# Kernel optimization log

Measured on AMD Instinct MI355X. Metric: run time of the kernel, lower is better.

Reference implementation:

```python
import jax, jax.numpy as jnp
import numpy as np

NUM_KIND = 4
V, Hh = 14, 6          # raw board
H, W = V - 2, Hh       # trimmed board 12x6
KS = 13                # full_kernel_size = max(12,6) -> odd 13
PAD = KS // 2
N_SQ = 100
LIN_IN = H * W         # 72


def _conv(x, w, b):
    # x: [N,1,H,W], w: [1,1,KS,KS], b: [1]
    y = jax.lax.conv_general_dilated(
        x, w, window_strides=(1, 1), padding=[(PAD, PAD), (PAD, PAD)],
        dimension_numbers=('NCHW', 'OIHW', 'NCHW'))
    return y + b[None, :, None, None]


def setup_inputs() -> dict:
    key = jax.random.key(0)
    ks = jax.random.split(key, 16)
    B = 65536
    dots = jax.random.randint(ks[0], (V, Hh, B), 0, NUM_KIND + 1, dtype=jnp.int32)
    std = 0.14
    def cw(k):
        return jax.random.normal(k, (1, 1, KS, KS), jnp.float32) * std
    def cb(k):
        return jax.random.normal(k, (1,), jnp.float32) * 0.05
    return {
        'dots_kind_matrix_3D': dots,
        'w_each': cw(ks[1]), 'b_each': cb(ks[2]),
        'w_not': cw(ks[3]), 'b_not': cb(ks[4]),
        'w_not2': cw(ks[5]), 'b_not2': cb(ks[6]),
        'w_empty': cw(ks[7]), 'b_empty': cb(ks[8]),
        'W1': jax.random.normal(ks[9], (N_SQ, LIN_IN), jnp.float32) * std,
        'b1': jax.random.normal(ks[10], (N_SQ,), jnp.float32) * 0.05,
        'W2': jax.random.normal(ks[11], (N_SQ, N_SQ), jnp.float32) * std,
        'b2': jax.random.normal(ks[12], (N_SQ,), jnp.float32) * 0.05,
        'W3': jax.random.normal(ks[13], (1, N_SQ), jnp.float32) * std,
        'b3': jax.random.normal(ks[14], (1,), jnp.float32) * 0.05,
    }


def _generate_linear_input(dots, w_each, b_each, w_not, b_not, w_not2, b_not2,
                           w_empty, b_empty):
    # trim last two rows, move batch axis first: [B,1,H,W]
    d = jnp.transpose(dots[:-2], (2, 0, 1))[:, None].astype(jnp.float32)
    B = d.shape[0]
    empty = _conv((d == 0).astype(jnp.float32), w_empty, b_empty)  # [B,1,H,W]

    # all kinds at once: masks [K,B,1,H,W]
    kinds = jnp.arange(1, NUM_KIND + 1, dtype=jnp.float32)
    masks = (d[None] == kinds[:, None, None, None, None]).astype(jnp.float32)

    mflat = masks.reshape(NUM_KIND * B, 1, H, W)
    ecv_log = _conv(mflat, w_each, b_each).reshape(NUM_KIND, B, 1, H, W)
    not_mat = jnp.where((masks + empty[None]) > 0, 0.0, 1.0)
    not_conv = _conv(not_mat.reshape(NUM_KIND * B, 1, H, W), w_not, b_not)
    not_conv = not_conv.reshape(NUM_KIND, B, 1, H, W)

    val = ecv_log + empty[None] - not_conv
    val = jnp.where(masks > 0, val, 0.0)
    all_color_value = jnp.sum(val, axis=0)  # [B,1,H,W]

    # second pass: sequential over kinds (carry feeds next iteration)
    def step(acv2, inp):
        ecm, ecv = inp  # [B,1,H,W]
        not2 = jnp.where((ecm + empty) > 0, 0.0, acv2)
        v = ecv + empty + _conv(not2, w_not2, b_not2)
        v = jnp.where(ecm > 0, v, 0.0)
        return acv2 + v, None

    acv2, _ = jax.lax.scan(step, all_color_value, (masks, ecv_log))
    return acv2.reshape(B, LIN_IN)


def reference(dots_kind_matrix_3D, w_each, b_each, w_not, b_not, w_not2, b_not2,
              w_empty, b_empty, W1, b1, W2, b2, W3, b3):
    x = _generate_linear_input(dots_kind_matrix_3D, w_each, b_each, w_not, b_not,
                               w_not2, b_not2, w_empty, b_empty)
    x = jax.nn.leaky_relu(x @ W1.T + b1, negative_slope=0.2)
    x = jax.nn.leaky_relu(x @ W2.T + b2, negative_slope=0.2)
    return x @ W3.T + b3  # [B,1]
```

## Files before the change

### kernel.cpp

```cpp
#include <hip/hip_runtime.h>

#define BN 65536
#define NT 256
#define NBB 64
#define NBLK (BN / NBB)

typedef unsigned int uint;
typedef unsigned short ushort;
typedef __attribute__((ext_vector_type(8))) short bf16x8;
typedef __attribute__((ext_vector_type(4))) float f32x4;

#define L_A  0
#define L_B  6400
#define L_B1 12800
#define L_B2 12912
#define L_W3 13024
#define L_TOT 13136

#define WS_W1 51200
#define WS_W2 69120
#define WS_TOT 94208
#define WS_MK_BYTE 188416

__device__ __forceinline__ uint f2b(float f){
  uint u = __float_as_uint(f);
  return (u + 0x7FFFu + ((u >> 16) & 1u)) >> 16;
}
__device__ __forceinline__ float b2f(uint h){ return __uint_as_float(h << 16); }
__device__ __forceinline__ uint dupb(float f){ uint b = f2b(f); return b | (b << 16); }

union BU { uint u[4]; bf16x8 v; };

__global__ __launch_bounds__(256) void k_setup(
    const float* __restrict__ w_each, const float* __restrict__ w_not,
    const float* __restrict__ w_not2, const float* __restrict__ w_empty,
    const float* __restrict__ W1, const float* __restrict__ W2,
    ushort* __restrict__ wsp)
{
  int id = blockIdx.x * 256 + threadIdx.x;
  if (id >= WS_TOT) return;
  float val = 0.f;
  int part;
  if (id < 51200) {
    int m = id / 12800, r = id % 12800;
    int fi = r >> 3, j = r & 7;
    int l = fi & 63, tk = fi >> 6;
    int ks = tk % 5, ti = tk / 5;
    int row = ti * 16 + (l & 15);
    int k = ks * 32 + (l >> 4) * 8 + j;
    int t = k >> 1; part = k & 1;
    if (row < 72 && t < 72) {
      int dr = t / 6 - row / 6 + 6, dc = t % 6 - row % 6 + 6;
      const float* w = m == 0 ? w_each : m == 1 ? w_not : m == 2 ? w_not2 : w_empty;
      if (dr >= 0 && dr < 13) val = w[dr * 13 + dc];
    }
  } else if (id < WS_W2) {
    int r = id - WS_W1;
    int fi = r >> 3, j = r & 7;
    int l = fi & 63, tk = fi >> 6;
    int ks = tk % 5, ti = tk / 5;
    int row = ti * 16 + (l & 15);
    int k = ks * 32 + (l >> 4) * 8 + j;
    int t = k >> 1; part = k & 1;
    if (row < 100 && t < 72) val = W1[row * 72 + t];
  } else {
    int r = id - WS_W2;
    int fi = r >> 3, j = r & 7;
    int l = fi & 63, tk = fi >> 6;
    int ks = tk % 7, ti = tk / 7;
    int row = ti * 16 + (l & 15);
    int k = ks * 32 + (l >> 4) * 8 + j;
    int t = k >> 1; part = k & 1;
    if (row < 100 && t < 100) val = W2[row * 100 + t];
  }
  uint h = f2b(val);
  if (part) { float rem = val - b2f(h); h = f2b(rem); }
  wsp[id] = (ushort)h;
}

__global__ __launch_bounds__(256) void k_masks(const int* __restrict__ dots,
                                               uint* __restrict__ MKg)
{
  int b = blockIdx.x * 256 + threadIdx.x;
  uint mk[5][3] = {};
#pragma unroll
  for (int c = 0; c < 72; ++c) {
    int v = dots[c * BN + b];
#pragma unroll
    for (int k = 0; k < 5; ++k)
      mk[k][c >> 5] |= (uint)(v == k) << (c & 31);
  }
#pragma unroll
  for (int k = 0; k < 5; ++k)
#pragma unroll
    for (int w = 0; w < 3; ++w)
      MKg[(k * 3 + w) * BN + b] = mk[k][w];
}

template<int NTK, int KW, int KS0, int NKS>
__device__ __forceinline__ void gstage(uint* afb, const ushort* __restrict__ wsp,
                                       int baseU16, int wid, int lane)
{
  const uint4* src = (const uint4*)(wsp + baseU16);
  constexpr int NIT = (NTK * 64 + NT - 1) / NT;
#pragma unroll
  for (int it = 0; it < NIT; ++it) {
    int tk = it * 4 + wid;
    if (tk < NTK) {
      int ksl = tk % NKS, ti = tk / NKS;
      const uint4* gp = src + (ti * KW + KS0 + ksl) * 64 + lane;
      uint4* lp = (uint4*)afb + tk * 64;
      __builtin_amdgcn_global_load_lds(
          (const __attribute__((address_space(1))) void*)gp,
          (__attribute__((address_space(3))) void*)lp, 16, 0, 0);
    }
  }
}

template<int NKS, int B0, int NBQ>
__device__ __forceinline__ void fcStep(const uint* sAF, const BU (&Bq)[NBQ],
                                       f32x4 (&Acc)[7], int lane)
{
  const bf16x8* AF = (const bf16x8*)sAF;
#pragma unroll
  for (int ti = 0; ti < 7; ++ti)
#pragma unroll
    for (int ksl = 0; ksl < NKS; ++ksl)
      Acc[ti] = __builtin_amdgcn_mfma_f32_16x16x32_bf16(
          AF[(ti * NKS + ksl) * 64 + lane], Bq[B0 + ksl].v, Acc[ti], 0, 0, 0);
}

__global__ __launch_bounds__(NT, 2) void k_main(
    const uint* __restrict__ MKg, const ushort* __restrict__ wsp,
    const float* __restrict__ b_each, const float* __restrict__ b_not,
    const float* __restrict__ b_not2, const float* __restrict__ b_empty,
    const float* __restrict__ b1, const float* __restrict__ b2,
    const float* __restrict__ W3, const float* __restrict__ b3,
    float* __restrict__ out)
{
  __shared__ uint sB[L_TOT];
  const int tid = threadIdx.x;
  const int wid = tid >> 6, lane = tid & 63;
  const int grp = lane >> 4;
  const int bl = wid * 16 + (lane & 15);
  const int gq = grp * 4;

  const float c_each = *b_each, c_not = *b_not, c_not2 = *b_not2, c_empty = *b_empty;
  const float c_b3 = *b3;

  if (tid < 112) {
    ((float*)(sB + L_B1))[tid] = (tid < 100) ? b1[tid] : 0.f;
    ((float*)(sB + L_B2))[tid] = (tid < 100) ? b2[tid] : 0.f;
    ((float*)(sB + L_W3))[tid] = (tid < 100) ? W3[tid] : 0.f;
  }
  gstage<25, 5, 0, 5>(sB + L_A, wsp, 3 * 12800, wid, lane);

  uint mkr[15];
  {
    const int gb = blockIdx.x * NBB + bl;
#pragma unroll
    for (int w = 0; w < 15; ++w) mkr[w] = MKg[w * BN + gb];
  }
  __syncthreads();

  f32x4 S5[5], A5[5];
  uint zws[5] = {0, 0, 0, 0, 0};

  gstage<25, 5, 0, 5>(sB + L_B, wsp, 0, wid, lane);
  {
    const bf16x8* AF = (const bf16x8*)(sB + L_A);
    BU Bv[5];
#pragma unroll
    for (int ks = 0; ks < 5; ++ks) {
      uint wv = mkr[0 * 3 + (ks >> 1)];
      int base = ((ks * 16) & 31) + gq;
#pragma unroll
      for (int q = 0; q < 4; ++q)
        Bv[ks].u[q] = ((wv >> (base + q)) & 1u) ? 0x3F803F80u : 0u;
    }
#pragma unroll
    for (int ti = 0; ti < 5; ++ti) {
      f32x4 d = {c_empty, c_empty, c_empty, c_empty};
#pragma unroll
      for (int ks = 0; ks < 5; ++ks)
        d = __builtin_amdgcn_mfma_f32_16x16x32_bf16(AF[(ti * 5 + ks) * 64 + lane], Bv[ks].v, d, 0, 0, 0);
      S5[ti] = d;
    }
  }
#pragma unroll
  for (int k = 1; k <= 4; ++k) {
#pragma unroll
    for (int ti = 0; ti < 5; ++ti) {
      uint wv = mkr[k * 3 + (ti >> 1)];
      int base = ((ti * 16) & 31) + gq;
#pragma unroll
      for (int r = 0; r < 4; ++r) {
        float mb = (float)((wv >> (base + r)) & 1u);
        if (S5[ti][r] + mb > 0.f) zws[ti] |= 1u << (r * 8 + (k - 1));
      }
    }
  }
  __syncthreads();

  gstage<25, 5, 0, 5>(sB + L_A, wsp, 1 * 12800, wid, lane);
  {
    const bf16x8* AF = (const bf16x8*)(sB + L_B);
#pragma unroll 1
    for (int k = 1; k <= 4; ++k) {
      BU Bv[5];
#pragma unroll
      for (int ks = 0; ks < 5; ++ks) {
        uint wv = mkr[k * 3 + (ks >> 1)];
        int base = ((ks * 16) & 31) + gq;
#pragma unroll
        for (int q = 0; q < 4; ++q)
          Bv[ks].u[q] = ((wv >> (base + q)) & 1u) ? 0x3F803F80u : 0u;
      }
#pragma unroll
      for (int ti = 0; ti < 5; ++ti) {
        f32x4 d = {c_each, c_each, c_each, c_each};
#pragma unroll
        for (int ks = 0; ks < 5; ++ks)
          d = __builtin_amdgcn_mfma_f32_16x16x32_bf16(AF[(ti * 5 + ks) * 64 + lane], Bv[ks].v, d, 0, 0, 0);
        uint wv = mkr[k * 3 + (ti >> 1)];
        int base = ((ti * 16) & 31) + gq;
#pragma unroll
        for (int r = 0; r < 4; ++r)
          if ((wv >> (base + r)) & 1u) S5[ti][r] += d[r];
      }
    }
  }
#pragma unroll
  for (int ti = 0; ti < 5; ++ti) {
    uint wv = mkr[0 * 3 + (ti >> 1)];
    int base = ((ti * 16) & 31) + gq;
#pragma unroll
    for (int r = 0; r < 4; ++r)
      A5[ti][r] = ((wv >> (base + r)) & 1u) ? 0.f : S5[ti][r];
  }
  __syncthreads();

  gstage<25, 5, 0, 5>(sB + L_B, wsp, 2 * 12800, wid, lane);
  {
    const bf16x8* AF = (const bf16x8*)(sB + L_A);
#pragma unroll 1
    for (int k = 1; k <= 4; ++k) {
      BU Bv[5];
#pragma unroll
      for (int ks = 0; ks < 5; ++ks) {
#pragma unroll
        for (int q = 0; q < 4; ++q)
          Bv[ks].u[q] = ((zws[ks] >> (q * 8 + (k - 1))) & 1u) ? 0u : 0x3F803F80u;
      }
#pragma unroll
      for (int ti = 0; ti < 5; ++ti) {
        f32x4 d = {c_not, c_not, c_not, c_not};
#pragma unroll
        for (int ks = 0; ks < 5; ++ks)
          d = __builtin_amdgcn_mfma_f32_16x16x32_bf16(AF[(ti * 5 + ks) * 64 + lane], Bv[ks].v, d, 0, 0, 0);
        uint wv = mkr[k * 3 + (ti >> 1)];
        int base = ((ti * 16) & 31) + gq;
#pragma unroll
        for (int r = 0; r < 4; ++r)
          if ((wv >> (base + r)) & 1u) A5[ti][r] -= d[r];
      }
    }
  }
  __syncthreads();

  gstage<21, 5, 0, 3>(sB + L_A, wsp, WS_W1, wid, lane);
  {
    const bf16x8* AF = (const bf16x8*)(sB + L_B);
#pragma unroll 1
    for (int k = 1; k <= 4; ++k) {
      BU Bv[5];
#pragma unroll
      for (int ks = 0; ks < 5; ++ks) {
#pragma unroll
        for (int q = 0; q < 4; ++q)
          Bv[ks].u[q] = ((zws[ks] >> (q * 8 + (k - 1))) & 1u) ? 0u : dupb(A5[ks][q]);
      }
#pragma unroll
      for (int ti = 0; ti < 5; ++ti) {
        f32x4 d = {c_not2, c_not2, c_not2, c_not2};
#pragma unroll
        for (int ks = 0; ks < 5; ++ks)
          d = __builtin_amdgcn_mfma_f32_16x16x32_bf16(AF[(ti * 5 + ks) * 64 + lane], Bv[ks].v, d, 0, 0, 0);
        uint wv = mkr[k * 3 + (ti >> 1)];
        int base = ((ti * 16) & 31) + gq;
#pragma unroll
        for (int r = 0; r < 4; ++r)
          if ((wv >> (base + r)) & 1u) A5[ti][r] += S5[ti][r] + d[r];
      }
    }
  }
  __syncthreads();

  BU Bx[5];
#pragma unroll
  for (int ks = 0; ks < 5; ++ks)
#pragma unroll
    for (int q = 0; q < 4; ++q) Bx[ks].u[q] = dupb(A5[ks][q]);
  f32x4 H[7];
#pragma unroll
  for (int ti = 0; ti < 7; ++ti) H[ti] = ((const f32x4*)(sB + L_B1))[ti * 4 + grp];

  gstage<14, 5, 3, 2>(sB + L_B, wsp, WS_W1, wid, lane);
  fcStep<3, 0>(sB + L_A, Bx, H, lane);
  __syncthreads();
  gstage<21, 7, 0, 3>(sB + L_A, wsp, WS_W2, wid, lane);
  fcStep<2, 3>(sB + L_B, Bx, H, lane);

  BU By[7];
#pragma unroll
  for (int ti = 0; ti < 7; ++ti) {
#pragma unroll
    for (int r = 0; r < 4; ++r) { float x = H[ti][r]; H[ti][r] = fmaxf(x, 0.2f * x); }
#pragma unroll
    for (int r = 0; r < 4; ++r) By[ti].u[r] = dupb(H[ti][r]);
  }
  f32x4 G[7];
#pragma unroll
  for (int ti = 0; ti < 7; ++ti) G[ti] = ((const f32x4*)(sB + L_B2))[ti * 4 + grp];
  __syncthreads();

  gstage<14, 7, 3, 2>(sB + L_B, wsp, WS_W2, wid, lane);
  fcStep<3, 0>(sB + L_A, By, G, lane);
  __syncthreads();
  gstage<14, 7, 5, 2>(sB + L_A, wsp, WS_W2, wid, lane);
  fcStep<2, 3>(sB + L_B, By, G, lane);
  __syncthreads();
  fcStep<2, 5>(sB + L_A, By, G, lane);

  float pd = 0.f;
#pragma unroll
  for (int ti = 0; ti < 7; ++ti) {
    f32x4 w3v = ((const f32x4*)(sB + L_W3))[ti * 4 + grp];
#pragma unroll
    for (int r = 0; r < 4; ++r) {
      float g = G[ti][r];
      g = fmaxf(g, 0.2f * g);
      pd = fmaf(w3v[r], g, pd);
    }
  }
  pd += __shfl_xor(pd, 16);
  pd += __shfl_xor(pd, 32);
  if (lane < 16) out[blockIdx.x * NBB + wid * 16 + lane] = pd + c_b3;
}

extern "C" void kernel_launch(void* const* d_in, const int* in_sizes, int n_in,
                              void* d_out, int out_size, void* d_ws, size_t ws_size,
                              hipStream_t stream)
{
  const int*   dots    = (const int*)d_in[0];
  const float* w_each  = (const float*)d_in[1];
  const float* b_each  = (const float*)d_in[2];
  const float* w_not   = (const float*)d_in[3];
  const float* b_not   = (const float*)d_in[4];
  const float* w_not2  = (const float*)d_in[5];
  const float* b_not2  = (const float*)d_in[6];
  const float* w_empty = (const float*)d_in[7];
  const float* b_empty = (const float*)d_in[8];
  const float* W1 = (const float*)d_in[9];
  const float* b1 = (const float*)d_in[10];
  const float* W2 = (const float*)d_in[11];
  const float* b2 = (const float*)d_in[12];
  const float* W3 = (const float*)d_in[13];
  const float* b3 = (const float*)d_in[14];

  (void)in_sizes; (void)n_in; (void)out_size; (void)ws_size;

  ushort* wsp = (ushort*)d_ws;
  uint*   MKg = (uint*)((char*)d_ws + WS_MK_BYTE);

  k_setup<<<(WS_TOT + 255) / 256, 256, 0, stream>>>(
      w_each, w_not, w_not2, w_empty, W1, W2, wsp);
  k_masks<<<BN / 256, 256, 0, stream>>>(dots, MKg);
  k_main<<<NBLK, NT, 0, stream>>>(
      MKg, wsp, b_each, b_not, b_not2, b_empty, b1, b2, W3, b3, (float*)d_out);
}
```

Measured before the change: 58.22 us.

## Merge prep kernels, skip structurally zero conv tiles, pair kinds, use hardware bf16 cvt

Fuses the weight-setup and mask-building kernels into one launch, removing a kernel launch and its gap. Skips MFMA calls for the two conv-weight tile blocks that are structurally zero given the 13x13 kernel on the 12x6 board. Processes kinds in pairs in the each-conv stage so each A fragment load feeds two MFMAs. Replaces the software round-to-nearest bf16 packing with the v_cvt_pk_bf16_f32 instruction, which may round slightly differently.

```diff
diff --git a/kernel.cpp b/kernel.cpp
--- a/kernel.cpp
+++ b/kernel.cpp
@@ -21,22 +21,47 @@
 #define WS_W2 69120
 #define WS_TOT 94208
 #define WS_MK_BYTE 188416
+#define SETUP_BLOCKS 368
+
+#define ZBLK(ti, ks) (((ti) == 0 && (ks) == 4) || ((ti) == 4 && (ks) == 0))
 
 __device__ __forceinline__ uint f2b(float f){
   uint u = __float_as_uint(f);
   return (u + 0x7FFFu + ((u >> 16) & 1u)) >> 16;
 }
 __device__ __forceinline__ float b2f(uint h){ return __uint_as_float(h << 16); }
-__device__ __forceinline__ uint dupb(float f){ uint b = f2b(f); return b | (b << 16); }
+__device__ __forceinline__ uint dup_cvt(float f){
+  uint r;
+  asm("v_cvt_pk_bf16_f32 %0, %1, %2" : "=v"(r) : "v"(f), "v"(f));
+  return r;
+}
 
 union BU { uint u[4]; bf16x8 v; };
 
-__global__ __launch_bounds__(256) void k_setup(
+__global__ __launch_bounds__(256) void k_prep(
     const float* __restrict__ w_each, const float* __restrict__ w_not,
     const float* __restrict__ w_not2, const float* __restrict__ w_empty,
     const float* __restrict__ W1, const float* __restrict__ W2,
-    ushort* __restrict__ wsp)
+    const int* __restrict__ dots,
+    ushort* __restrict__ wsp, uint* __restrict__ MKg)
 {
+  if (blockIdx.x >= SETUP_BLOCKS) {
+    int b = (blockIdx.x - SETUP_BLOCKS) * 256 + threadIdx.x;
+    uint mk[5][3] = {};
+#pragma unroll
+    for (int c = 0; c < 72; ++c) {
+      int v = dots[c * BN + b];
+#pragma unroll
+      for (int k = 0; k < 5; ++k)
+        mk[k][c >> 5] |= (uint)(v == k) << (c & 31);
+    }
+#pragma unroll
+    for (int k = 0; k < 5; ++k)
+#pragma unroll
+      for (int w = 0; w < 3; ++w)
+        MKg[(k * 3 + w) * BN + b] = mk[k][w];
+    return;
+  }
   int id = blockIdx.x * 256 + threadIdx.x;
   if (id >= WS_TOT) return;
   float val = 0.f;
@@ -78,25 +103,6 @@
   wsp[id] = (ushort)h;
 }
 
-__global__ __launch_bounds__(256) void k_masks(const int* __restrict__ dots,
-                                               uint* __restrict__ MKg)
-{
-  int b = blockIdx.x * 256 + threadIdx.x;
-  uint mk[5][3] = {};
-#pragma unroll
-  for (int c = 0; c < 72; ++c) {
-    int v = dots[c * BN + b];
-#pragma unroll
-    for (int k = 0; k < 5; ++k)
-      mk[k][c >> 5] |= (uint)(v == k) << (c & 31);
-  }
-#pragma unroll
-  for (int k = 0; k < 5; ++k)
-#pragma unroll
-    for (int w = 0; w < 3; ++w)
-      MKg[(k * 3 + w) * BN + b] = mk[k][w];
-}
-
 template<int NTK, int KW, int KS0, int NKS>
 __device__ __forceinline__ void gstage(uint* afb, const ushort* __restrict__ wsp,
                                        int baseU16, int wid, int lane)
@@ -182,8 +188,10 @@
     for (int ti = 0; ti < 5; ++ti) {
       f32x4 d = {c_empty, c_empty, c_empty, c_empty};
 #pragma unroll
-      for (int ks = 0; ks < 5; ++ks)
+      for (int ks = 0; ks < 5; ++ks) {
+        if (ZBLK(ti, ks)) continue;
         d = __builtin_amdgcn_mfma_f32_16x16x32_bf16(AF[(ti * 5 + ks) * 64 + lane], Bv[ks].v, d, 0, 0, 0);
+      }
       S5[ti] = d;
     }
   }
@@ -206,27 +214,43 @@
   {
     const bf16x8* AF = (const bf16x8*)(sB + L_B);
 #pragma unroll 1
-    for (int k = 1; k <= 4; ++k) {
-      BU Bv[5];
+    for (int kp = 0; kp < 2; ++kp) {
+      const int k0 = 2 * kp + 1, k1 = 2 * kp + 2;
+      f32x4 d0[5], d1[5];
+#pragma unroll
+      for (int ti = 0; ti < 5; ++ti) {
+        d0[ti] = (f32x4){c_each, c_each, c_each, c_each};
+        d1[ti] = (f32x4){c_each, c_each, c_each, c_each};
+      }
 #pragma unroll
       for (int ks = 0; ks < 5; ++ks) {
-        uint wv = mkr[k * 3 + (ks >> 1)];
+        BU B0, B1;
+        uint wv0 = mkr[k0 * 3 + (ks >> 1)];
+        uint wv1 = mkr[k1 * 3 + (ks >> 1)];
         int base = ((ks * 16) & 31) + gq;
 #pragma unroll
-        for (int q = 0; q < 4; ++q)
-          Bv[ks].u[q] = ((wv >> (base + q)) & 1u) ? 0x3F803F80u : 0u;
+        for (int q = 0; q < 4; ++q) {
+          B0.u[q] = ((wv0 >> (base + q)) & 1u) ? 0x3F803F80u : 0u;
+          B1.u[q] = ((wv1 >> (base + q)) & 1u) ? 0x3F803F80u : 0u;
+        }
+#pragma unroll
+        for (int ti = 0; ti < 5; ++ti) {
+          if (ZBLK(ti, ks)) continue;
+          bf16x8 a = AF[(ti * 5 + ks) * 64 + lane];
+          d0[ti] = __builtin_amdgcn_mfma_f32_16x16x32_bf16(a, B0.v, d0[ti], 0, 0, 0);
+          d1[ti] = __builtin_amdgcn_mfma_f32_16x16x32_bf16(a, B1.v, d1[ti], 0, 0, 0);
+        }
       }
 #pragma unroll
       for (int ti = 0; ti < 5; ++ti) {
-        f32x4 d = {c_each, c_each, c_each, c_each};
-#pragma unroll
-        for (int ks = 0; ks < 5; ++ks)
-          d = __builtin_amdgcn_mfma_f32_16x16x32_bf16(AF[(ti * 5 + ks) * 64 + lane], Bv[ks].v, d, 0, 0, 0);
-        uint wv = mkr[k * 3 + (ti >> 1)];
+        uint wv0 = mkr[k0 * 3 + (ti >> 1)];
+        uint wv1 = mkr[k1 * 3 + (ti >> 1)];
         int base = ((ti * 16) & 31) + gq;
 #pragma unroll
-        for (int r = 0; r < 4; ++r)
-          if ((wv >> (base + r)) & 1u) S5[ti][r] += d[r];
+        for (int r = 0; r < 4; ++r) {
+          if ((wv0 >> (base + r)) & 1u) S5[ti][r] += d0[ti][r];
+          if ((wv1 >> (base + r)) & 1u) S5[ti][r] += d1[ti][r];
+        }
       }
     }
   }
@@ -256,8 +280,10 @@
       for (int ti = 0; ti < 5; ++ti) {
         f32x4 d = {c_not, c_not, c_not, c_not};
 #pragma unroll
-        for (int ks = 0; ks < 5; ++ks)
+        for (int ks = 0; ks < 5; ++ks) {
+          if (ZBLK(ti, ks)) continue;
           d = __builtin_amdgcn_mfma_f32_16x16x32_bf16(AF[(ti * 5 + ks) * 64 + lane], Bv[ks].v, d, 0, 0, 0);
+        }
         uint wv = mkr[k * 3 + (ti >> 1)];
         int base = ((ti * 16) & 31) + gq;
 #pragma unroll
@@ -278,14 +304,16 @@
       for (int ks = 0; ks < 5; ++ks) {
 #pragma unroll
         for (int q = 0; q < 4; ++q)
-          Bv[ks].u[q] = ((zws[ks] >> (q * 8 + (k - 1))) & 1u) ? 0u : dupb(A5[ks][q]);
+          Bv[ks].u[q] = ((zws[ks] >> (q * 8 + (k - 1))) & 1u) ? 0u : dup_cvt(A5[ks][q]);
       }
 #pragma unroll
       for (int ti = 0; ti < 5; ++ti) {
         f32x4 d = {c_not2, c_not2, c_not2, c_not2};
 #pragma unroll
-        for (int ks = 0; ks < 5; ++ks)
+        for (int ks = 0; ks < 5; ++ks) {
+          if (ZBLK(ti, ks)) continue;
           d = __builtin_amdgcn_mfma_f32_16x16x32_bf16(AF[(ti * 5 + ks) * 64 + lane], Bv[ks].v, d, 0, 0, 0);
+        }
         uint wv = mkr[k * 3 + (ti >> 1)];
         int base = ((ti * 16) & 31) + gq;
 #pragma unroll
@@ -300,7 +328,7 @@
 #pragma unroll
   for (int ks = 0; ks < 5; ++ks)
 #pragma unroll
-    for (int q = 0; q < 4; ++q) Bx[ks].u[q] = dupb(A5[ks][q]);
+    for (int q = 0; q < 4; ++q) Bx[ks].u[q] = dup_cvt(A5[ks][q]);
   f32x4 H[7];
 #pragma unroll
   for (int ti = 0; ti < 7; ++ti) H[ti] = ((const f32x4*)(sB + L_B1))[ti * 4 + grp];
@@ -317,7 +345,7 @@
 #pragma unroll
     for (int r = 0; r < 4; ++r) { float x = H[ti][r]; H[ti][r] = fmaxf(x, 0.2f * x); }
 #pragma unroll
-    for (int r = 0; r < 4; ++r) By[ti].u[r] = dupb(H[ti][r]);
+    for (int r = 0; r < 4; ++r) By[ti].u[r] = dup_cvt(H[ti][r]);
   }
   f32x4 G[7];
 #pragma unroll
@@ -373,9 +401,8 @@
   ushort* wsp = (ushort*)d_ws;
   uint*   MKg = (uint*)((char*)d_ws + WS_MK_BYTE);
 
-  k_setup<<<(WS_TOT + 255) / 256, 256, 0, stream>>>(
-      w_each, w_not, w_not2, w_empty, W1, W2, wsp);
-  k_masks<<<BN / 256, 256, 0, stream>>>(dots, MKg);
+  k_prep<<<SETUP_BLOCKS + BN / 256, 256, 0, stream>>>(
+      w_each, w_not, w_not2, w_empty, W1, W2, dots, wsp, MKg);
   k_main<<<NBLK, NT, 0, stream>>>(
       MKg, wsp, b_each, b_not, b_not2, b_empty, b1, b2, W3, b3, (float*)d_out);
 }
```

After: 53.97 us. 7.3% less time.
